# Kernel tuning notes

Hardware: AMD Instinct MI355X
Metric: run time of the kernel (lower is better)

Reference implementation:

```python
import jax, jax.numpy as jnp
import numpy as np


def setup_inputs() -> dict:
    key = jax.random.key(0)
    ks = jax.random.split(key, 5)
    B, C, H, W = 4, 256, 48, 48
    x = jax.random.normal(ks[0], (B, C, H, W), dtype=jnp.float32)
    w_qkv = jax.random.normal(ks[1], (3 * C, C), dtype=jnp.float32) * (C ** -0.5)
    b_qkv = jax.random.normal(ks[2], (3 * C,), dtype=jnp.float32) * 0.02
    w_proj = jax.random.normal(ks[3], (C, C), dtype=jnp.float32) * (C ** -0.5)
    b_proj = jax.random.normal(ks[4], (C,), dtype=jnp.float32) * 0.02
    return {"x": x, "w_qkv": w_qkv, "b_qkv": b_qkv, "w_proj": w_proj, "b_proj": b_proj, "num_heads": 4}


def reference(x, w_qkv, b_qkv, w_proj, b_proj, num_heads):
    B, C, H, W = x.shape
    N = H * W
    hd = C // num_heads
    # NOTE: original uses full-dim scale, not head_dim
    scale = C ** -0.5
    # 1x1 conv == channel matmul
    qkv = jnp.einsum('bchw,oc->bohw', x, w_qkv) + b_qkv[None, :, None, None]
    qkv = qkv.reshape(B, 3, num_heads, hd, N)
    q = qkv[:, 0].transpose(0, 1, 3, 2)  # [B, h, N, d]
    k = qkv[:, 1]                         # [B, h, d, N]
    v = qkv[:, 2].transpose(0, 1, 3, 2)  # [B, h, N, d]
    attn = jax.nn.softmax((q @ k) * scale, axis=-1)  # [B, h, N, N]
    out = attn @ v                        # [B, h, N, d]
    out = out.transpose(0, 1, 3, 2).reshape(B, C, H, W)
    return jnp.einsum('bchw,oc->bohw', out, w_proj) + b_proj[None, :, None, None]
```

## Files before the change

kernel.cpp:

```cpp
#include <hip/hip_runtime.h>
#include <hip/hip_bf16.h>
#include <stdint.h>

typedef unsigned short u16;
typedef unsigned int u32;
typedef __attribute__((ext_vector_type(8))) short bf16x8;
typedef __attribute__((ext_vector_type(4))) float f32x4;
typedef __attribute__((ext_vector_type(4))) unsigned short u16x4;

#define MFMA16 __builtin_amdgcn_mfma_f32_16x16x32_bf16

static constexpr int Bb = 4;
static constexpr int Cc = 256;
static constexpr int NHh = 4;
static constexpr int HDd = 64;
static constexpr int Nn = 2304;

__device__ __forceinline__ u16 f2bf(float f) {
  u32 u = __builtin_bit_cast(u32, f);
  u32 r = u + 0x7fffu + ((u >> 16) & 1u);
  return (u16)(r >> 16);
}

__device__ __forceinline__ u32 cvtpk(float a, float b) {
  u32 r;
  asm("v_cvt_pk_bf16_f32 %0, %1, %2" : "=v"(r) : "v"(a), "v"(b));
  return r;
}

__device__ __forceinline__ void async16(const void* g, void* l) {
  __builtin_amdgcn_global_load_lds(
      (const __attribute__((address_space(1))) u32*)g,
      (__attribute__((address_space(3))) u32*)l, 16, 0, 0);
}

__global__ __launch_bounds__(256) void k_prep(const float* __restrict__ wq,
                                              const float* __restrict__ wp,
                                              const float* __restrict__ x,
                                              u16* __restrict__ wqb,
                                              u16* __restrict__ wpb,
                                              u16* __restrict__ xT) {
  __shared__ float tile[64][65];
  int bx = blockIdx.x;
  if (bx < 768) {
    int i = bx * 256 + threadIdx.x;
    if (i < 3 * Cc * Cc) wqb[i] = f2bf(wq[i]);
    if (i < Cc * Cc)     wpb[i] = f2bf(wp[i]);
    return;
  }
  int t2 = bx - 768;
  int c0 = (t2 & 3) * 64, n0 = ((t2 >> 2) % 36) * 64, b = (t2 >> 2) / 36;
  int w = threadIdx.x >> 6, lane = threadIdx.x & 63;
#pragma unroll
  for (int i = 0; i < 16; ++i) {
    int c = i * 4 + w;
    tile[c][lane] = x[((size_t)(b * Cc + c0 + c)) * Nn + n0 + lane];
  }
  __syncthreads();
#pragma unroll
  for (int i = 0; i < 16; ++i) {
    int n = i * 4 + w;
    xT[((size_t)(b * Nn + n0 + n)) * Cc + c0 + lane] = f2bf(tile[lane][n]);
  }
}

__global__ __launch_bounds__(256) void k_qkv(const u16* __restrict__ wqb,
                                             const u16* __restrict__ xT,
                                             const float* __restrict__ bqkv,
                                             u16* __restrict__ qT, u16* __restrict__ kT,
                                             u16* __restrict__ vT) {
  __shared__ u16 Bs[64 * 256];
  int n0 = blockIdx.y * 64, b = blockIdx.z;
  int t = threadIdx.x, w = t >> 6, l = t & 63, g = l >> 4, li = l & 15;
#pragma unroll
  for (int it = 0; it < 8; ++it) {
    int ch = it * 256 + t;
    int row = ch >> 5, c16 = ch & 31;
    const char* src = (const char*)xT + ((size_t)(b * Nn + n0 + row)) * 512 +
                      ((c16 * 16) ^ ((row & 7) << 4));
    async16(src, (char*)Bs + (it * 256 + (t & ~63)) * 16);
  }
  __syncthreads();
  const float qs = 0.0625f * 1.44269504088896340736f;
#pragma unroll
  for (int p = 0; p < 2; ++p) {
    int o0 = blockIdx.x * 128 + p * 64;
    const u16* Arow = wqb + (size_t)(o0 + w * 16 + li) * Cc;
    f32x4 acc[4] = {};
#pragma unroll
    for (int s = 0; s < 8; ++s) {
      bf16x8 a = *(const bf16x8*)(Arow + s * 32 + g * 8);
#pragma unroll
      for (int nt = 0; nt < 4; ++nt) {
        int row = nt * 16 + li;
        const char* bp_ = (const char*)Bs + row * 512 + ((s * 64 + g * 16) ^ ((row & 7) << 4));
        bf16x8 bb = *(const bf16x8*)bp_;
        acc[nt] = MFMA16(a, bb, acc[nt], 0, 0, 0);
      }
    }
    int which = o0 >> 8;
    int hh = (o0 >> 6) & 3;
    int bh = b * NHh + hh;
    int dbase = w * 16 + g * 4;
#pragma unroll
    for (int nt = 0; nt < 4; ++nt) {
      int n = n0 + nt * 16 + li;
      float v0 = acc[nt][0] + bqkv[o0 + dbase + 0];
      float v1 = acc[nt][1] + bqkv[o0 + dbase + 1];
      float v2 = acc[nt][2] + bqkv[o0 + dbase + 2];
      float v3 = acc[nt][3] + bqkv[o0 + dbase + 3];
      if (which == 0) {
        u16x4 pq = {f2bf(v0 * qs), f2bf(v1 * qs), f2bf(v2 * qs), f2bf(v3 * qs)};
        *(u16x4*)(qT + ((size_t)bh * Nn + n) * HDd + dbase) = pq;
      } else if (which == 1) {
        u16x4 pk = {f2bf(v0), f2bf(v1), f2bf(v2), f2bf(v3)};
        *(u16x4*)(kT + ((size_t)bh * Nn + n) * HDd + dbase) = pk;
      } else {
        vT[((size_t)bh * HDd + dbase + 0) * Nn + n] = f2bf(v0);
        vT[((size_t)bh * HDd + dbase + 1) * Nn + n] = f2bf(v1);
        vT[((size_t)bh * HDd + dbase + 2) * Nn + n] = f2bf(v2);
        vT[((size_t)bh * HDd + dbase + 3) * Nn + n] = f2bf(v3);
      }
    }
  }
}

__global__ __launch_bounds__(192) void k_attn(const u16* __restrict__ qT,
                                              const u16* __restrict__ kT,
                                              const u16* __restrict__ vT,
                                              u16* __restrict__ attP,
                                              float* __restrict__ lsumP) {
  __shared__ u16 Ks[2][32 * 64];
  __shared__ u16 Vs[2][64 * 32];
  __shared__ u16 Ps[3][16 * 64];
  int L = blockIdx.x;
  int xcd = L & 7, r = L >> 3;
  int bh = 2 * xcd + (r >= 96 ? 1 : 0);
  int rr = (r >= 96) ? r - 96 : r;
  int half = (rr >= 48) ? 1 : 0;
  int qb = (rr >= 48) ? rr - 48 : rr;
  int t = threadIdx.x, w = t / 64, l = t & 63, g = l >> 4, li = l & 15;
  int q0 = qb * 48 + w * 16;
  const u16* qrow = qT + ((size_t)bh * Nn + q0 + li) * HDd;
  bf16x8 bq0 = *(const bf16x8*)(qrow + g * 8);
  bf16x8 bq1 = *(const bf16x8*)(qrow + 32 + g * 8);
  const short one = (short)0x3F80;
  bf16x8 ONES = {one, one, one, one, one, one, one, one};
  f32x4 acc[4] = {};
  f32x4 acc_l = {};
  const char* kbh = (const char*)(kT + (size_t)bh * Nn * HDd);
  const char* vbh = (const char*)(vT + (size_t)bh * HDd * Nn);
  char* PsB = (char*)(&Ps[w][0]);
  int sw_li = (li & 7) << 4;
  int sw_v  = (li & 3) << 4;

  const char* sp[3];
  int sd[3], sstr[3];
  bool son[3], svv[3];
#pragma unroll
  for (int it = 0; it < 3; ++it) {
    int gg = w * 3 + it;
    son[it] = (gg < 8);
    int c = gg * 64 + l;
    if (c < 256) {
      int key = c >> 3, c8 = c & 7;
      sp[it] = kbh + (size_t)(half * 1152 + key) * 128 + ((c8 * 16) ^ ((key & 7) << 4));
      sd[it] = c * 16; sstr[it] = 32 * 128; svv[it] = false;
    } else {
      int cv = c - 256, d = cv >> 2, c4 = cv & 3;
      sp[it] = vbh + (size_t)d * (Nn * 2) + half * 2304 + ((c4 * 16) ^ ((d & 3) << 4));
      sd[it] = cv * 16; sstr[it] = 32 * 2; svv[it] = true;
    }
  }

  auto STAGE = [&](int buf) {
    char* kdst = (char*)(&Ks[0][0]) + buf * 4096;
    char* vdst = (char*)(&Vs[0][0]) + buf * 4096;
#pragma unroll
    for (int it = 0; it < 3; ++it) {
      if (son[it]) {
        async16(sp[it], (svv[it] ? vdst : kdst) + sd[it]);
        sp[it] += sstr[it];
      }
    }
  };

  STAGE(0);
  int cur = 0;
  for (int kb = 0; kb < 36; ++kb) {
    __syncthreads();
    if (kb + 1 < 36) STAGE(cur ^ 1);

    const char* Kc = (const char*)(&Ks[0][0]) + cur * 4096;
    const char* Vc = (const char*)(&Vs[0][0]) + cur * 4096;

    f32x4 s[2];
    __builtin_amdgcn_s_setprio(1);
#pragma unroll
    for (int kt = 0; kt < 2; ++kt) {
      const char* kr = Kc + (kt * 16 + li) * 128;
      bf16x8 a0 = *(const bf16x8*)(kr + ((g * 16) ^ sw_li));
      bf16x8 a1 = *(const bf16x8*)(kr + ((64 + g * 16) ^ sw_li));
      f32x4 z = {};
      z = MFMA16(a0, bq0, z, 0, 0, 0);
      z = MFMA16(a1, bq1, z, 0, 0, 0);
      s[kt] = z;
    }
    __builtin_amdgcn_s_setprio(0);

#pragma unroll
    for (int kt = 0; kt < 2; ++kt)
#pragma unroll
      for (int rr2 = 0; rr2 < 4; ++rr2) s[kt][rr2] = exp2f(s[kt][rr2]);

#pragma unroll
    for (int kt = 0; kt < 2; ++kt) {
      uint2 pk;
      pk.x = cvtpk(s[kt][0], s[kt][1]);
      pk.y = cvtpk(s[kt][2], s[kt][3]);
      *(uint2*)(PsB + li * 128 + ((kt * 32 + g * 8) ^ sw_li)) = pk;
    }
    bf16x8 pa0 = *(const bf16x8*)(PsB + li * 128 + ((g * 16) ^ sw_li));
    __builtin_amdgcn_s_setprio(1);
    acc_l = MFMA16(pa0, ONES, acc_l, 0, 0, 0);
#pragma unroll
    for (int dt = 0; dt < 4; ++dt) {
      const char* vr = Vc + (dt * 16 + li) * 64;
      bf16x8 v0 = *(const bf16x8*)(vr + ((g * 16) ^ sw_v));
      acc[dt] = MFMA16(pa0, v0, acc[dt], 0, 0, 0);
    }
    __builtin_amdgcn_s_setprio(0);
    cur ^= 1;
  }
  u16* ap = attP + (size_t)half * (Bb * Nn * Cc);
  float* lp = lsumP + half * (Bb * NHh * Nn);
  if (li == 0) {
#pragma unroll
    for (int rr2 = 0; rr2 < 4; ++rr2) lp[bh * Nn + q0 + g * 4 + rr2] = acc_l[rr2];
  }
  int b = bh >> 2, hh = bh & 3;
#pragma unroll
  for (int dt = 0; dt < 4; ++dt) {
    int cidx = hh * 64 + dt * 16 + li;
#pragma unroll
    for (int rr2 = 0; rr2 < 4; ++rr2) {
      ap[((size_t)(b * Nn + q0 + g * 4 + rr2)) * Cc + cidx] = f2bf(acc[dt][rr2]);
    }
  }
}

__global__ __launch_bounds__(256) void k_proj(const u16* __restrict__ wpb,
                                              const u16* __restrict__ attP,
                                              const float* __restrict__ lsumP,
                                              const float* __restrict__ bp,
                                              float* __restrict__ out) {
  __shared__ u16 Bs[2][32 * 256];
  int o0 = blockIdx.x * 64, n0 = blockIdx.y * 32, b = blockIdx.z;
  int t = threadIdx.x, w = t >> 6, l = t & 63, g = l >> 4, li = l & 15;
#pragma unroll
  for (int it = 0; it < 8; ++it) {
    int ch = it * 256 + t;
    int hf = ch >> 10, rem = ch & 1023;
    int row = rem >> 5, c16 = rem & 31;
    const char* src = (const char*)(attP + (size_t)hf * (Bb * Nn * Cc)) +
                      ((size_t)(b * Nn + n0 + row)) * 512 +
                      ((c16 * 16) ^ ((row & 7) << 4));
    async16(src, (char*)Bs + (it * 256 + (t & ~63)) * 16);
  }
  const u16* Arow = wpb + (size_t)(o0 + w * 16 + li) * Cc;
  __syncthreads();
  f32x4 acc[4][2] = {};
#pragma unroll
  for (int s = 0; s < 8; ++s) {
    bf16x8 a = *(const bf16x8*)(Arow + s * 32 + g * 8);
#pragma unroll
    for (int hf = 0; hf < 2; ++hf) {
#pragma unroll
      for (int nt = 0; nt < 2; ++nt) {
        int row = nt * 16 + li;
        const char* bp_ = (const char*)Bs + hf * (32 * 512) + row * 512 +
                          ((s * 64 + g * 16) ^ ((row & 7) << 4));
        bf16x8 bb = *(const bf16x8*)bp_;
        acc[s >> 1][nt] = MFMA16(a, bb, acc[s >> 1][nt], 0, 0, 0);
      }
    }
  }
  int obase = o0 + w * 16 + g * 4;
#pragma unroll
  for (int nt = 0; nt < 2; ++nt) {
    int n = n0 + nt * 16 + li;
    float inv[4];
#pragma unroll
    for (int h = 0; h < 4; ++h) {
      int lidx = (b * NHh + h) * Nn + n;
      inv[h] = 1.0f / (lsumP[lidx] + lsumP[Bb * NHh * Nn + lidx]);
    }
#pragma unroll
    for (int rr2 = 0; rr2 < 4; ++rr2) {
      float v = acc[0][nt][rr2] * inv[0] + acc[1][nt][rr2] * inv[1] +
                acc[2][nt][rr2] * inv[2] + acc[3][nt][rr2] * inv[3];
      out[((size_t)(b * Cc + obase + rr2)) * Nn + n] = v + bp[obase + rr2];
    }
  }
}

extern "C" void kernel_launch(void* const* d_in, const int* in_sizes, int n_in,
                              void* d_out, int out_size, void* d_ws, size_t ws_size,
                              hipStream_t stream) {
  const float* x     = (const float*)d_in[0];
  const float* wqkv  = (const float*)d_in[1];
  const float* bqkv  = (const float*)d_in[2];
  const float* wproj = (const float*)d_in[3];
  const float* bproj = (const float*)d_in[4];
  float* out = (float*)d_out;

  u16* ws    = (u16*)d_ws;
  u16* wq_bf = ws;
  u16* wp_bf = wq_bf + 196608;
  u16* xT    = wp_bf + 65536;
  u16* qT    = xT + 2359296;
  u16* kT    = qT + 2359296;
  u16* vT    = kT + 2359296;
  u16* attP  = vT + 2359296;
  float* lsumP = (float*)(attP + 2 * 2359296);

  k_prep<<<dim3(1344), dim3(256), 0, stream>>>(wqkv, wproj, x, wq_bf, wp_bf, xT);
  k_qkv<<<dim3(6, 36, 4), dim3(256), 0, stream>>>(wq_bf, xT, bqkv, qT, kT, vT);
  k_attn<<<dim3(1536), dim3(192), 0, stream>>>(qT, kT, vT, attP, lsumP);
  k_proj<<<dim3(4, 72, 4), dim3(256), 0, stream>>>(wp_bf, attP, lsumP, bproj, out);
}
```

Measured before the change: 84.60 us.

## Split attention keys into quarters with 32 queries per wave, widen projection tiles

Each attention wave now processes 32 query rows instead of 16, so every staged K/V tile is reused twice. Each block covers a quarter of the key sequence rather than half, which halves the loop length per block. The P scratch and the V swizzle are adapted to 32-wide rows. The projection kernel now reduces four partial attention outputs and four partial row sums, computes 128 output channels per block to reuse the staged tiles, and aliases xT onto the attP buffer to save workspace. This raises register pressure and adds extra partial-sum traffic and reduction work in the projection.

```diff
diff --git a/kernel.cpp b/kernel.cpp
--- a/kernel.cpp
+++ b/kernel.cpp
@@ -132,30 +132,35 @@
                                               float* __restrict__ lsumP) {
   __shared__ u16 Ks[2][32 * 64];
   __shared__ u16 Vs[2][64 * 32];
-  __shared__ u16 Ps[3][16 * 64];
+  __shared__ u16 Ps[3][32 * 32];
   int L = blockIdx.x;
   int xcd = L & 7, r = L >> 3;
   int bh = 2 * xcd + (r >= 96 ? 1 : 0);
-  int rr = (r >= 96) ? r - 96 : r;
-  int half = (rr >= 48) ? 1 : 0;
-  int qb = (rr >= 48) ? rr - 48 : rr;
+  int r2 = (r >= 96) ? r - 96 : r;
+  int quarter = r2 / 24;
+  int qb = r2 % 24;
   int t = threadIdx.x, w = t / 64, l = t & 63, g = l >> 4, li = l & 15;
-  int q0 = qb * 48 + w * 16;
-  const u16* qrow = qT + ((size_t)bh * Nn + q0 + li) * HDd;
-  bf16x8 bq0 = *(const bf16x8*)(qrow + g * 8);
-  bf16x8 bq1 = *(const bf16x8*)(qrow + 32 + g * 8);
+  int q0 = qb * 96 + w * 32;
+  const u16* qr0 = qT + ((size_t)bh * Nn + q0 + li) * HDd;
+  const u16* qr1 = qT + ((size_t)bh * Nn + q0 + 16 + li) * HDd;
+  bf16x8 bq[2][2];
+  bq[0][0] = *(const bf16x8*)(qr0 + g * 8);
+  bq[0][1] = *(const bf16x8*)(qr0 + 32 + g * 8);
+  bq[1][0] = *(const bf16x8*)(qr1 + g * 8);
+  bq[1][1] = *(const bf16x8*)(qr1 + 32 + g * 8);
   const short one = (short)0x3F80;
   bf16x8 ONES = {one, one, one, one, one, one, one, one};
-  f32x4 acc[4] = {};
-  f32x4 acc_l = {};
+  f32x4 acc[2][4] = {};
+  f32x4 acc_l[2] = {};
   const char* kbh = (const char*)(kT + (size_t)bh * Nn * HDd);
   const char* vbh = (const char*)(vT + (size_t)bh * HDd * Nn);
   char* PsB = (char*)(&Ps[w][0]);
   int sw_li = (li & 7) << 4;
-  int sw_v  = (li & 3) << 4;
+  int sw2   = ((li >> 1) & 3) << 4;
 
   const char* sp[3];
-  int sd[3], sstr[3];
+  int sd[3];
+  ptrdiff_t sstr[3];
   bool son[3], svv[3];
 #pragma unroll
   for (int it = 0; it < 3; ++it) {
@@ -164,11 +169,12 @@
     int c = gg * 64 + l;
     if (c < 256) {
       int key = c >> 3, c8 = c & 7;
-      sp[it] = kbh + (size_t)(half * 1152 + key) * 128 + ((c8 * 16) ^ ((key & 7) << 4));
+      sp[it] = kbh + (size_t)(quarter * 576 + key) * 128 + ((c8 * 16) ^ ((key & 7) << 4));
       sd[it] = c * 16; sstr[it] = 32 * 128; svv[it] = false;
     } else {
       int cv = c - 256, d = cv >> 2, c4 = cv & 3;
-      sp[it] = vbh + (size_t)d * (Nn * 2) + half * 2304 + ((c4 * 16) ^ ((d & 3) << 4));
+      sp[it] = vbh + (size_t)d * (Nn * 2) + quarter * 1152 +
+               ((c4 * 16) ^ (((d >> 1) & 3) << 4));
       sd[it] = cv * 16; sstr[it] = 32 * 2; svv[it] = true;
     }
   }
@@ -187,66 +193,81 @@
 
   STAGE(0);
   int cur = 0;
-  for (int kb = 0; kb < 36; ++kb) {
+  for (int kb = 0; kb < 18; ++kb) {
     __syncthreads();
-    if (kb + 1 < 36) STAGE(cur ^ 1);
+    if (kb + 1 < 18) STAGE(cur ^ 1);
 
     const char* Kc = (const char*)(&Ks[0][0]) + cur * 4096;
     const char* Vc = (const char*)(&Vs[0][0]) + cur * 4096;
 
-    f32x4 s[2];
+    f32x4 s[2][2];
     __builtin_amdgcn_s_setprio(1);
 #pragma unroll
     for (int kt = 0; kt < 2; ++kt) {
       const char* kr = Kc + (kt * 16 + li) * 128;
       bf16x8 a0 = *(const bf16x8*)(kr + ((g * 16) ^ sw_li));
       bf16x8 a1 = *(const bf16x8*)(kr + ((64 + g * 16) ^ sw_li));
-      f32x4 z = {};
-      z = MFMA16(a0, bq0, z, 0, 0, 0);
-      z = MFMA16(a1, bq1, z, 0, 0, 0);
-      s[kt] = z;
+#pragma unroll
+      for (int st = 0; st < 2; ++st) {
+        f32x4 z = {};
+        z = MFMA16(a0, bq[st][0], z, 0, 0, 0);
+        z = MFMA16(a1, bq[st][1], z, 0, 0, 0);
+        s[st][kt] = z;
+      }
     }
     __builtin_amdgcn_s_setprio(0);
 
 #pragma unroll
-    for (int kt = 0; kt < 2; ++kt)
-#pragma unroll
-      for (int rr2 = 0; rr2 < 4; ++rr2) s[kt][rr2] = exp2f(s[kt][rr2]);
-
-#pragma unroll
-    for (int kt = 0; kt < 2; ++kt) {
-      uint2 pk;
-      pk.x = cvtpk(s[kt][0], s[kt][1]);
-      pk.y = cvtpk(s[kt][2], s[kt][3]);
-      *(uint2*)(PsB + li * 128 + ((kt * 32 + g * 8) ^ sw_li)) = pk;
-    }
-    bf16x8 pa0 = *(const bf16x8*)(PsB + li * 128 + ((g * 16) ^ sw_li));
+    for (int st = 0; st < 2; ++st) {
+#pragma unroll
+      for (int kt = 0; kt < 2; ++kt)
+#pragma unroll
+        for (int j = 0; j < 4; ++j) s[st][kt][j] = exp2f(s[st][kt][j]);
+      int rq = st * 16 + li;
+#pragma unroll
+      for (int kt = 0; kt < 2; ++kt) {
+        uint2 pk;
+        pk.x = cvtpk(s[st][kt][0], s[st][kt][1]);
+        pk.y = cvtpk(s[st][kt][2], s[st][kt][3]);
+        *(uint2*)(PsB + rq * 64 + ((kt * 32 + g * 8) ^ sw2)) = pk;
+      }
+    }
+    bf16x8 pa[2];
+    pa[0] = *(const bf16x8*)(PsB + (0 * 16 + li) * 64 + ((g * 16) ^ sw2));
+    pa[1] = *(const bf16x8*)(PsB + (1 * 16 + li) * 64 + ((g * 16) ^ sw2));
     __builtin_amdgcn_s_setprio(1);
-    acc_l = MFMA16(pa0, ONES, acc_l, 0, 0, 0);
+    acc_l[0] = MFMA16(pa[0], ONES, acc_l[0], 0, 0, 0);
+    acc_l[1] = MFMA16(pa[1], ONES, acc_l[1], 0, 0, 0);
 #pragma unroll
     for (int dt = 0; dt < 4; ++dt) {
       const char* vr = Vc + (dt * 16 + li) * 64;
-      bf16x8 v0 = *(const bf16x8*)(vr + ((g * 16) ^ sw_v));
-      acc[dt] = MFMA16(pa0, v0, acc[dt], 0, 0, 0);
+      bf16x8 v0 = *(const bf16x8*)(vr + ((g * 16) ^ sw2));
+      acc[0][dt] = MFMA16(pa[0], v0, acc[0][dt], 0, 0, 0);
+      acc[1][dt] = MFMA16(pa[1], v0, acc[1][dt], 0, 0, 0);
     }
     __builtin_amdgcn_s_setprio(0);
     cur ^= 1;
   }
-  u16* ap = attP + (size_t)half * (Bb * Nn * Cc);
-  float* lp = lsumP + half * (Bb * NHh * Nn);
+  u16* ap = attP + (size_t)quarter * (Bb * Nn * Cc);
+  float* lp = lsumP + quarter * (Bb * NHh * Nn);
   if (li == 0) {
 #pragma unroll
-    for (int rr2 = 0; rr2 < 4; ++rr2) lp[bh * Nn + q0 + g * 4 + rr2] = acc_l[rr2];
+    for (int st = 0; st < 2; ++st)
+#pragma unroll
+      for (int j = 0; j < 4; ++j)
+        lp[bh * Nn + q0 + st * 16 + g * 4 + j] = acc_l[st][j];
   }
   int b = bh >> 2, hh = bh & 3;
 #pragma unroll
-  for (int dt = 0; dt < 4; ++dt) {
-    int cidx = hh * 64 + dt * 16 + li;
-#pragma unroll
-    for (int rr2 = 0; rr2 < 4; ++rr2) {
-      ap[((size_t)(b * Nn + q0 + g * 4 + rr2)) * Cc + cidx] = f2bf(acc[dt][rr2]);
-    }
-  }
+  for (int st = 0; st < 2; ++st)
+#pragma unroll
+    for (int dt = 0; dt < 4; ++dt) {
+      int cidx = hh * 64 + dt * 16 + li;
+#pragma unroll
+      for (int j = 0; j < 4; ++j) {
+        ap[((size_t)(b * Nn + q0 + st * 16 + g * 4 + j)) * Cc + cidx] = f2bf(acc[st][dt][j]);
+      }
+    }
 }
 
 __global__ __launch_bounds__(256) void k_proj(const u16* __restrict__ wpb,
@@ -254,38 +275,40 @@
                                               const float* __restrict__ lsumP,
                                               const float* __restrict__ bp,
                                               float* __restrict__ out) {
-  __shared__ u16 Bs[2][32 * 256];
-  int o0 = blockIdx.x * 64, n0 = blockIdx.y * 32, b = blockIdx.z;
+  __shared__ u16 Bs[4][32 * 256];
+  int bx = blockIdx.x, n0 = blockIdx.y * 32, b = blockIdx.z;
   int t = threadIdx.x, w = t >> 6, l = t & 63, g = l >> 4, li = l & 15;
 #pragma unroll
-  for (int it = 0; it < 8; ++it) {
+  for (int it = 0; it < 16; ++it) {
     int ch = it * 256 + t;
-    int hf = ch >> 10, rem = ch & 1023;
+    int qtr = ch >> 10, rem = ch & 1023;
     int row = rem >> 5, c16 = rem & 31;
-    const char* src = (const char*)(attP + (size_t)hf * (Bb * Nn * Cc)) +
+    const char* src = (const char*)(attP + (size_t)qtr * (Bb * Nn * Cc)) +
                       ((size_t)(b * Nn + n0 + row)) * 512 +
                       ((c16 * 16) ^ ((row & 7) << 4));
     async16(src, (char*)Bs + (it * 256 + (t & ~63)) * 16);
   }
-  const u16* Arow = wpb + (size_t)(o0 + w * 16 + li) * Cc;
+  const u16* Arow0 = wpb + (size_t)(bx * 128 + w * 16 + li) * Cc;
+  const u16* Arow1 = Arow0 + (size_t)64 * Cc;
   __syncthreads();
-  f32x4 acc[4][2] = {};
+  f32x4 acc[2][4][2] = {};
 #pragma unroll
   for (int s = 0; s < 8; ++s) {
-    bf16x8 a = *(const bf16x8*)(Arow + s * 32 + g * 8);
-#pragma unroll
-    for (int hf = 0; hf < 2; ++hf) {
+    bf16x8 a0 = *(const bf16x8*)(Arow0 + s * 32 + g * 8);
+    bf16x8 a1 = *(const bf16x8*)(Arow1 + s * 32 + g * 8);
+#pragma unroll
+    for (int qtr = 0; qtr < 4; ++qtr) {
 #pragma unroll
       for (int nt = 0; nt < 2; ++nt) {
         int row = nt * 16 + li;
-        const char* bp_ = (const char*)Bs + hf * (32 * 512) + row * 512 +
+        const char* bp_ = (const char*)Bs + qtr * (32 * 512) + row * 512 +
                           ((s * 64 + g * 16) ^ ((row & 7) << 4));
         bf16x8 bb = *(const bf16x8*)bp_;
-        acc[s >> 1][nt] = MFMA16(a, bb, acc[s >> 1][nt], 0, 0, 0);
-      }
-    }
-  }
-  int obase = o0 + w * 16 + g * 4;
+        acc[0][s >> 1][nt] = MFMA16(a0, bb, acc[0][s >> 1][nt], 0, 0, 0);
+        acc[1][s >> 1][nt] = MFMA16(a1, bb, acc[1][s >> 1][nt], 0, 0, 0);
+      }
+    }
+  }
 #pragma unroll
   for (int nt = 0; nt < 2; ++nt) {
     int n = n0 + nt * 16 + li;
@@ -293,13 +316,19 @@
 #pragma unroll
     for (int h = 0; h < 4; ++h) {
       int lidx = (b * NHh + h) * Nn + n;
-      inv[h] = 1.0f / (lsumP[lidx] + lsumP[Bb * NHh * Nn + lidx]);
-    }
-#pragma unroll
-    for (int rr2 = 0; rr2 < 4; ++rr2) {
-      float v = acc[0][nt][rr2] * inv[0] + acc[1][nt][rr2] * inv[1] +
-                acc[2][nt][rr2] * inv[2] + acc[3][nt][rr2] * inv[3];
-      out[((size_t)(b * Cc + obase + rr2)) * Nn + n] = v + bp[obase + rr2];
+      float sum = lsumP[lidx] + lsumP[1 * Bb * NHh * Nn + lidx] +
+                  lsumP[2 * Bb * NHh * Nn + lidx] + lsumP[3 * Bb * NHh * Nn + lidx];
+      inv[h] = 1.0f / sum;
+    }
+#pragma unroll
+    for (int p = 0; p < 2; ++p) {
+      int obase = bx * 128 + p * 64 + w * 16 + g * 4;
+#pragma unroll
+      for (int j = 0; j < 4; ++j) {
+        float v = acc[p][0][nt][j] * inv[0] + acc[p][1][nt][j] * inv[1] +
+                  acc[p][2][nt][j] * inv[2] + acc[p][3][nt][j] * inv[3];
+        out[((size_t)(b * Cc + obase + j)) * Nn + n] = v + bp[obase + j];
+      }
     }
   }
 }
@@ -317,15 +346,15 @@
   u16* ws    = (u16*)d_ws;
   u16* wq_bf = ws;
   u16* wp_bf = wq_bf + 196608;
-  u16* xT    = wp_bf + 65536;
-  u16* qT    = xT + 2359296;
+  u16* qT    = wp_bf + 65536;
   u16* kT    = qT + 2359296;
   u16* vT    = kT + 2359296;
   u16* attP  = vT + 2359296;
-  float* lsumP = (float*)(attP + 2 * 2359296);
+  u16* xT    = attP;
+  float* lsumP = (float*)(attP + 4 * 2359296);
 
   k_prep<<<dim3(1344), dim3(256), 0, stream>>>(wqkv, wproj, x, wq_bf, wp_bf, xT);
   k_qkv<<<dim3(6, 36, 4), dim3(256), 0, stream>>>(wq_bf, xT, bqkv, qT, kT, vT);
   k_attn<<<dim3(1536), dim3(192), 0, stream>>>(qT, kT, vT, attP, lsumP);
-  k_proj<<<dim3(4, 72, 4), dim3(256), 0, stream>>>(wp_bf, attP, lsumP, bproj, out);
-}
+  k_proj<<<dim3(2, 72, 4), dim3(256), 0, stream>>>(wp_bf, attP, lsumP, bproj, out);
+}
```

Result: no change. 84.31 us (-0.3%).
